# Kernel optimization log

Hardware: AMD Instinct MI355X
Metric: run time of the kernel (lower is better)

The kernel has to match this reference:

```python
import jax, jax.numpy as jnp
import numpy as np
import math

NH, NR, HD, QK, ITERS = 8, 8, 64, 32, 4


def _pe(seq_len, dim):
    n = 1.0 / (1.0 + math.exp(-1))
    pos = np.arange(seq_len, dtype=np.float64)[:, None]
    i = np.arange(0, dim, 2, dtype=np.float64)[None, :]
    pe = np.zeros((seq_len, dim), np.float32)
    pe[:, 0::2] = n * np.sin(pos / 10000 ** (2 * i / dim))
    pe[:, 1::2] = n * np.cos(pos / 10000 ** (2 * (i + 1) / dim))
    return jnp.asarray(pe)


def _ln(x, g, b, eps=1e-5):
    m = x.mean(-1, keepdims=True)
    v = ((x - m) ** 2).mean(-1, keepdims=True)
    return (x - m) * jax.lax.rsqrt(v + eps) * g + b


def _comp_attn(x, norm1_g, norm1_b, norm2_g, norm2_b, q_w, q_b, k_w, k_b,
               v_w, v_b, qv_w, qv_b, score_w, score_b, final_w, final_b,
               ffn1_w, ffn1_b, ffn2_w, ffn2_b):
    B, S, D = x.shape
    res = x
    h = _ln(x, norm1_g, norm1_b)
    q = (h @ q_w + q_b).reshape(B, S, NH, HD).transpose(0, 2, 1, 3) / math.sqrt(HD)  # [B,nh,S,hd]
    k = (h @ k_w + k_b).reshape(B, S, NH, HD)                                         # [B,S,nh,hd]
    v = (h @ v_w + v_b).reshape(B, S, NR, HD)                                         # [B,S,nr,hd]
    score = jax.nn.softmax(jnp.einsum('bhqd,bkhd->bhqk', q, k), axis=-1)              # [B,nh,S,S]
    out = jnp.einsum('bhqk,bkrd->bqhrd', score, v)                                    # [B,S,nh,nr,hd]
    qv = (h @ qv_w + qv_b).reshape(B, S, NH, QK)
    qv_e = jnp.broadcast_to(qv[:, :, :, None, :], (B, S, NH, NR, QK))
    in_ = jnp.concatenate([qv_e, out], axis=-1)                                       # [B,S,nh,nr,qk+hd]
    comp = jax.nn.softmax(in_ @ score_w + score_b, axis=3)                            # [B,S,nh,nr,1]
    o = (comp * out).sum(axis=3).reshape(B, S, D)
    o = o @ final_w + final_b
    x = res + o
    res2 = x
    h2 = _ln(x, norm2_g, norm2_b)
    ff = jax.nn.relu(h2 @ ffn1_w + ffn1_b) @ ffn2_w + ffn2_b  # dropout identity (eval)
    return res2 + ff


def reference(img, qst, conv_w, conv_b, qrep_w, qrep_b, cls_token, map_w, map_b,
              norm1_g, norm1_b, norm2_g, norm2_b, q_w, q_b, k_w, k_b, v_w, v_b,
              qv_w, qv_b, score_w, score_b, final_w, final_b,
              ffn1_w, ffn1_b, ffn2_w, ffn2_b, out_w, out_b):
    B = img.shape[0]
    H = conv_w.shape[0]  # 256
    pe = _pe(25, H)
    # patch embedding: conv 15x15 stride 15 -> [B,H,5,5]
    p = jax.lax.conv_general_dilated(img, conv_w, (15, 15), 'VALID',
                                     dimension_numbers=('NCHW', 'OIHW', 'NCHW'))
    p = p + conv_b[None, :, None, None]
    p = p.reshape(B, H, 25).transpose(0, 2, 1) + pe[None]       # [B,25,H]
    cls = jnp.broadcast_to(cls_token, (B, 1, H))
    emb = jnp.concatenate([cls, p], axis=1)                      # [B,26,H]
    que = (qst @ qrep_w + qrep_b)[:, None, :]
    que = jnp.broadcast_to(que, (B, 26, H))
    x = jnp.concatenate([emb, que], axis=-1)                     # [B,26,2H]
    x = x @ map_w + map_b                                        # [B,26,D]
    for _ in range(ITERS):
        x = _comp_attn(x, norm1_g, norm1_b, norm2_g, norm2_b, q_w, q_b, k_w, k_b,
                       v_w, v_b, qv_w, qv_b, score_w, score_b, final_w, final_b,
                       ffn1_w, ffn1_b, ffn2_w, ffn2_b)
    y = x[:, 0, :] @ out_w + out_b
    return jax.nn.log_softmax(y, axis=1)


def setup_inputs() -> dict:
    key = jax.random.key(0)
    ks = iter(jax.random.split(key, 64))
    def rn(shape, s=0.02):
        return jax.random.normal(next(ks), shape, jnp.float32) * s
    B, D, H = 256, 512, 256
    return {
        'img': jax.random.normal(next(ks), (B, 3, 75, 75), jnp.float32),
        'qst': jax.random.normal(next(ks), (B, 18), jnp.float32),
        'conv_w': rn((H, 3, 15, 15)), 'conv_b': rn((H,)),
        'qrep_w': rn((18, H)), 'qrep_b': rn((H,)),
        'cls_token': rn((1, 1, H), 1.0),
        'map_w': rn((2 * H, D)), 'map_b': rn((D,)),
        'norm1_g': jnp.ones((D,), jnp.float32), 'norm1_b': jnp.zeros((D,), jnp.float32),
        'norm2_g': jnp.ones((D,), jnp.float32), 'norm2_b': jnp.zeros((D,), jnp.float32),
        'q_w': rn((D, D)), 'q_b': rn((D,)),
        'k_w': rn((D, D)), 'k_b': rn((D,)),
        'v_w': rn((D, NR * HD)), 'v_b': rn((NR * HD,)),
        'qv_w': rn((D, QK * NH)), 'qv_b': rn((QK * NH,)),
        'score_w': rn((HD + QK, 1)), 'score_b': rn((1,)),
        'final_w': rn((D, D)), 'final_b': rn((D,)),
        'ffn1_w': rn((D, 2 * D)), 'ffn1_b': rn((2 * D,)),
        'ffn2_w': rn((2 * D, D)), 'ffn2_b': rn((D,)),
        'out_w': rn((D, 10)), 'out_b': rn((10,)),
    }
```

## Files before the change

kernel.cpp:

```cpp
#include <hip/hip_runtime.h>
#include <math.h>

#define NB 256
#define SEQ 26
#define TOK (NB*SEQ)
#define DIM 512

typedef unsigned short u16;
typedef __attribute__((ext_vector_type(8))) short short8_t;
typedef __attribute__((ext_vector_type(4))) float floatx4;

__device__ inline u16 f2bf(float f) {
    union { float f; unsigned u; } v; v.f = f;
    unsigned r = v.u + 0x7fffu + ((v.u >> 16) & 1u);
    return (u16)(r >> 16);
}
__device__ inline float bf2f(u16 u) {
    union { unsigned u; float f; } v; v.u = ((unsigned)u) << 16; return v.f;
}

__device__ __forceinline__ void gload_lds16(const u16* g, u16* l) {
    __builtin_amdgcn_global_load_lds((const __attribute__((address_space(1))) void*)g,
                                     (__attribute__((address_space(3))) void*)l, 16, 0, 0);
}

__global__ void prep_all(const float* __restrict__ q_w, const float* __restrict__ k_w,
                         const float* __restrict__ v_w, const float* __restrict__ final_w,
                         const float* __restrict__ ffn1_w, const float* __restrict__ ffn2_w,
                         const float* __restrict__ map_w, const float* __restrict__ conv_w,
                         const float* __restrict__ q_b, const float* __restrict__ k_b,
                         const float* __restrict__ v_b, const float* __restrict__ cls,
                         const float* __restrict__ qst, const float* __restrict__ qrep_w,
                         const float* __restrict__ qrep_b, const float* __restrict__ map_b,
                         u16* __restrict__ qkvT, u16* __restrict__ finT,
                         u16* __restrict__ f1T, u16* __restrict__ f2T,
                         u16* __restrict__ mapT, u16* __restrict__ cwT,
                         float* __restrict__ qkvb, u16* __restrict__ emb,
                         float* __restrict__ quem) {
    __shared__ float lds[64][65];
    __shared__ float que[256];
    int blk = blockIdx.x;
    int t = threadIdx.x;
    if (blk < 544) {
        const float* W; u16* Wt; int K, N, tbase;
        if (blk < 64)       { W = q_w;     Wt = qkvT;            K = 512;  N = 512;  tbase = 0;   }
        else if (blk < 128) { W = k_w;     Wt = qkvT + 512*512;  K = 512;  N = 512;  tbase = 64;  }
        else if (blk < 192) { W = v_w;     Wt = qkvT + 1024*512; K = 512;  N = 512;  tbase = 128; }
        else if (blk < 256) { W = final_w; Wt = finT;            K = 512;  N = 512;  tbase = 192; }
        else if (blk < 384) { W = ffn1_w;  Wt = f1T;             K = 512;  N = 1024; tbase = 256; }
        else if (blk < 512) { W = ffn2_w;  Wt = f2T;             K = 1024; N = 512;  tbase = 384; }
        else                { W = map_w;   Wt = mapT;            K = 256;  N = 512;  tbase = 512; }
        int tloc = blk - tbase;
        int ntn = N >> 6;
        int n0 = (tloc % ntn) * 64, k0 = (tloc / ntn) * 64;
        int j = t & 63, i0 = t >> 6;
        #pragma unroll
        for (int p = 0; p < 16; ++p) {
            int i = i0*16 + p;
            lds[i][j] = W[(size_t)(k0+i)*N + n0 + j];
        }
        __syncthreads();
        int i2 = t & 63, j0 = t >> 6;
        #pragma unroll
        for (int p = 0; p < 16; ++p) {
            int j2 = j0*16 + p;
            Wt[(size_t)(n0+j2)*K + k0 + i2] = f2bf(lds[i2][j2]);
        }
    } else if (blk < 800) {
        int oc = blk - 544;
        for (int jj = t; jj < 704; jj += 256)
            cwT[(size_t)oc*704 + jj] = (jj < 675) ? f2bf(conv_w[(size_t)oc*675 + jj]) : (u16)0;
    } else if (blk < 1056) {
        int b = blk - 800;
        emb[(size_t)(b*SEQ)*256 + t] = f2bf(cls[t]);
    } else if (blk == 1056) {
        for (int jj = t; jj < 1536; jj += 256)
            qkvb[jj] = jj < 512 ? q_b[jj] : (jj < 1024 ? k_b[jj-512] : v_b[jj-1024]);
    } else {
        int b = blk - 1057;
        float acc = qrep_b[t];
        for (int j = 0; j < 18; ++j) acc += qst[b*18 + j] * qrep_w[j*256 + t];
        que[t] = acc;
        __syncthreads();
        for (int n = t; n < DIM; n += 256) {
            float a2 = map_b[n];
            for (int k = 0; k < 256; ++k) a2 += que[k] * map_w[(256 + k)*DIM + n];
            quem[b*DIM + n] = a2;
        }
    }
}

__global__ void im2col_kernel(const float* __restrict__ img, u16* __restrict__ P) {
    int ri = blockIdx.x;
    int b = ri / 25, pos = ri % 25, ph = pos/5, pw = pos%5;
    for (int j = threadIdx.x; j < 704; j += 256) {
        float v = 0.f;
        if (j < 675) {
            int c = j / 225, rem = j % 225, kh = rem/15, kw = rem%15;
            v = img[(size_t)((b*3+c)*75 + ph*15 + kh)*75 + pw*15 + kw];
        }
        P[(size_t)ri*704 + j] = f2bf(v);
    }
}

template<int BM, int RESMODE, int RELU, int OUTBF>
__global__ __launch_bounds__(512) void mfma_gemm(const u16* __restrict__ A, const u16* __restrict__ Bt,
                          const float* __restrict__ bias, const void* __restrict__ res,
                          void* __restrict__ Cout, int M, int N, int K, float alpha) {
    constexpr int MI  = BM / 32;
    constexpr int ALD = BM / 64;
    __shared__ __align__(16) u16 As[2][BM*64];
    __shared__ __align__(16) u16 Bs[2][128*64];
    const int tid = threadIdx.x;
    const int lane = tid & 63;
    const int w = tid >> 6;
    const int wr = (w >> 2) * (MI*16);
    const int wc = (w & 3) * 32;
    const int bm = blockIdx.y * BM, bn = blockIdx.x * 128;

    floatx4 acc[MI][2];
    #pragma unroll
    for (int mi = 0; mi < MI; ++mi)
        #pragma unroll
        for (int ni = 0; ni < 2; ++ni)
            acc[mi][ni] = (floatx4){0.f,0.f,0.f,0.f};

    const u16* aptr[ALD];
    int aidx[ALD];
    #pragma unroll
    for (int s = 0; s < ALD; ++s) {
        int idx = s*512 + tid;
        int row = idx >> 3, ch = (idx & 7) ^ (row & 7);
        aptr[s] = &A[(size_t)(bm+row)*K + ch*8];
        aidx[s] = idx;
    }
    const u16* bptr[2];
    int bidx[2];
    #pragma unroll
    for (int s = 0; s < 2; ++s) {
        int idx = s*512 + tid;
        int row = idx >> 3, ch = (idx & 7) ^ (row & 7);
        bptr[s] = &Bt[(size_t)(bn+row)*K + ch*8];
        bidx[s] = idx;
    }

    const int nt = K >> 6;
    #pragma unroll
    for (int s = 0; s < ALD; ++s) gload_lds16(aptr[s], &As[0][aidx[s]*8]);
    #pragma unroll
    for (int s = 0; s < 2; ++s)   gload_lds16(bptr[s], &Bs[0][bidx[s]*8]);
    __syncthreads();

    for (int t = 0; t < nt; ++t) {
        const int cur = t & 1;
        if (t + 1 < nt) {
            int off = (t + 1) << 6;
            #pragma unroll
            for (int s = 0; s < ALD; ++s) gload_lds16(aptr[s] + off, &As[cur^1][aidx[s]*8]);
            #pragma unroll
            for (int s = 0; s < 2; ++s)   gload_lds16(bptr[s] + off, &Bs[cur^1][bidx[s]*8]);
        }
        #pragma unroll
        for (int kk = 0; kk < 2; ++kk) {
            int ch2 = kk*4 + (lane >> 4);
            short8_t af[MI], bf[2];
            #pragma unroll
            for (int mi = 0; mi < MI; ++mi) {
                int row = wr + mi*16 + (lane & 15);
                af[mi] = *(const short8_t*)&As[cur][row*64 + ((ch2 ^ (row & 7))*8)];
            }
            #pragma unroll
            for (int ni = 0; ni < 2; ++ni) {
                int rowb = wc + ni*16 + (lane & 15);
                bf[ni] = *(const short8_t*)&Bs[cur][rowb*64 + ((ch2 ^ (rowb & 7))*8)];
            }
            #pragma unroll
            for (int mi = 0; mi < MI; ++mi)
                #pragma unroll
                for (int ni = 0; ni < 2; ++ni)
                    acc[mi][ni] = __builtin_amdgcn_mfma_f32_16x16x32_bf16(
                        af[mi], bf[ni], acc[mi][ni], 0, 0, 0);
        }
        __syncthreads();
    }

    #pragma unroll
    for (int mi = 0; mi < MI; ++mi) {
        #pragma unroll
        for (int ni = 0; ni < 2; ++ni) {
            int col = bn + wc + ni*16 + (lane & 15);
            float bv = bias ? bias[col] : 0.0f;
            #pragma unroll
            for (int r = 0; r < 4; ++r) {
                int row = bm + wr + mi*16 + (lane >> 4)*4 + r;
                float v = (acc[mi][ni][r] + bv) * alpha;
                if (RELU) v = fmaxf(v, 0.f);
                if (RESMODE == 1)      v += bf2f(((const u16*)res)[(size_t)row*N + col]);
                else if (RESMODE == 2) v += ((const float*)res)[(size_t)(row/SEQ)*N + col];
                if (RESMODE == 3) {
                    int bb = row / 25, pos = row - bb*25;
                    float freq = __powf(10000.0f, -(float)col / 128.0f);
                    float a = (float)pos * freq;
                    float pe = 0.7310585786300049f * ((col & 1) ? __cosf(a) : __sinf(a));
                    ((u16*)Cout)[(size_t)(bb*SEQ + 1 + pos)*256 + col] = f2bf(v + pe);
                } else if (OUTBF) {
                    ((u16*)Cout)[(size_t)row*N + col] = f2bf(v);
                } else {
                    ((float*)Cout)[(size_t)row*N + col] = v;
                }
            }
        }
    }
}

__global__ void ln_kernel(const u16* __restrict__ x, const float* __restrict__ g,
                          const float* __restrict__ bta, u16* __restrict__ out) {
    int row = blockIdx.x * 4 + (threadIdx.x >> 6);
    int lane = threadIdx.x & 63;
    short8_t xin = *(const short8_t*)&x[(size_t)row*DIM + lane*8];
    float xv[8];
    #pragma unroll
    for (int j = 0; j < 8; ++j) xv[j] = bf2f((u16)xin[j]);
    float s = 0.f, sq = 0.f;
    #pragma unroll
    for (int j = 0; j < 8; ++j) { s += xv[j]; sq += xv[j]*xv[j]; }
    #pragma unroll
    for (int off = 32; off; off >>= 1) {
        s  += __shfl_xor(s,  off);
        sq += __shfl_xor(sq, off);
    }
    float m = s * (1.0f/DIM);
    float r = rsqrtf(sq * (1.0f/DIM) - m*m + 1e-5f);
    floatx4 g0 = *(const floatx4*)(g + lane*8);
    floatx4 g1 = *(const floatx4*)(g + lane*8 + 4);
    floatx4 b0 = *(const floatx4*)(bta + lane*8);
    floatx4 b1 = *(const floatx4*)(bta + lane*8 + 4);
    short8_t o;
    o[0] = (short)f2bf((xv[0]-m)*r*g0[0] + b0[0]);
    o[1] = (short)f2bf((xv[1]-m)*r*g0[1] + b0[1]);
    o[2] = (short)f2bf((xv[2]-m)*r*g0[2] + b0[2]);
    o[3] = (short)f2bf((xv[3]-m)*r*g0[3] + b0[3]);
    o[4] = (short)f2bf((xv[4]-m)*r*g1[0] + b1[0]);
    o[5] = (short)f2bf((xv[5]-m)*r*g1[1] + b1[1]);
    o[6] = (short)f2bf((xv[6]-m)*r*g1[2] + b1[2]);
    o[7] = (short)f2bf((xv[7]-m)*r*g1[3] + b1[3]);
    *(short8_t*)&out[(size_t)row*DIM + lane*8] = o;
}

__global__ __launch_bounds__(512) void attn_fused_kernel(const u16* __restrict__ qkv,
                                                         const float* __restrict__ score_w,
                                                         u16* __restrict__ attn_o) {
    int b = blockIdx.x;
    __shared__ u16 Bt[64*224];
    __shared__ float s_lds[208*28];
    __shared__ float vwl[208];
    __shared__ float cmp_lds[208*8];
    __shared__ float swl[64];
    int tid = threadIdx.x;
    int lane = tid & 63, w = tid >> 6;

    if (tid < 64) swl[tid] = score_w[32 + tid];
    for (int k = 0; k < 26; ++k) {
        int d2 = tid & 63, r = tid >> 6;
        u16 v = qkv[(size_t)(b*SEQ+k)*1536 + 1024 + tid];
        int bo = (d2*448 + (k*8+r)*2) ^ ((d2 & 7) << 4);
        *(u16*)((char*)Bt + bo) = v;
    }
    {
        int d2 = tid & 63, kr = 208 + (tid >> 6);
        int bo1 = (d2*448 + kr*2)     ^ ((d2 & 7) << 4);
        int bo2 = (d2*448 + (kr+8)*2) ^ ((d2 & 7) << 4);
        *(u16*)((char*)Bt + bo1) = 0;
        *(u16*)((char*)Bt + bo2) = 0;
    }
    for (int row = tid; row < 208; row += 512) {
        s_lds[row*28 + 26] = 0.f; s_lds[row*28 + 27] = 0.f;
    }

    {
        int h = w;
        int col16 = lane & 15, ch = lane >> 4;
        short8_t qf[2][2], kf[2][2];
        #pragma unroll
        for (int mi = 0; mi < 2; ++mi) {
            int q = mi*16 + col16;
            #pragma unroll
            for (int kk = 0; kk < 2; ++kk) {
                if (q < 26)
                    qf[mi][kk] = *(const short8_t*)&qkv[(size_t)(b*SEQ+q)*1536 + h*64 + kk*32 + ch*8];
                else
                    qf[mi][kk] = (short8_t){0,0,0,0,0,0,0,0};
            }
        }
        #pragma unroll
        for (int ni = 0; ni < 2; ++ni) {
            int kq = ni*16 + col16;
            #pragma unroll
            for (int kk = 0; kk < 2; ++kk) {
                if (kq < 26)
                    kf[ni][kk] = *(const short8_t*)&qkv[(size_t)(b*SEQ+kq)*1536 + 512 + h*64 + kk*32 + ch*8];
                else
                    kf[ni][kk] = (short8_t){0,0,0,0,0,0,0,0};
            }
        }
        floatx4 sacc[2][2];
        #pragma unroll
        for (int mi = 0; mi < 2; ++mi)
            #pragma unroll
            for (int ni = 0; ni < 2; ++ni)
                sacc[mi][ni] = (floatx4){0.f,0.f,0.f,0.f};
        #pragma unroll
        for (int kk = 0; kk < 2; ++kk)
            #pragma unroll
            for (int mi = 0; mi < 2; ++mi)
                #pragma unroll
                for (int ni = 0; ni < 2; ++ni)
                    sacc[mi][ni] = __builtin_amdgcn_mfma_f32_16x16x32_bf16(
                        qf[mi][kk], kf[ni][kk], sacc[mi][ni], 0, 0, 0);
        #pragma unroll
        for (int mi = 0; mi < 2; ++mi) {
            #pragma unroll
            for (int r = 0; r < 4; ++r) {
                float s0 = sacc[mi][0][r] * 0.125f;
                float s1 = (col16 < 10) ? sacc[mi][1][r] * 0.125f : -1e30f;
                float mx = fmaxf(s0, s1);
                #pragma unroll
                for (int msk = 1; msk < 16; msk <<= 1) mx = fmaxf(mx, __shfl_xor(mx, msk));
                float e0 = __expf(s0 - mx);
                float e1 = (col16 < 10) ? __expf(s1 - mx) : 0.f;
                float den = e0 + e1;
                #pragma unroll
                for (int msk = 1; msk < 16; msk <<= 1) den += __shfl_xor(den, msk);
                float inv = 1.f / den;
                int q = mi*16 + ch*4 + r;
                if (q < 26) {
                    s_lds[(h*26+q)*28 + col16] = e0 * inv;
                    if (col16 < 10) s_lds[(h*26+q)*28 + 16 + col16] = e1 * inv;
                }
            }
        }
    }
    __syncthreads();

    if (tid < 416) {
        int kr = tid >> 1, h0 = (tid & 1) * 32;
        float acc = 0.f;
        #pragma unroll
        for (int dd = 0; dd < 32; ++dd) {
            int d2 = h0 + dd;
            int bo = (d2*448 + kr*2) ^ ((d2 & 7) << 4);
            acc += bf2f(*(const u16*)((const char*)Bt + bo)) * swl[d2];
        }
        acc += __shfl_xor(acc, 1);
        if ((tid & 1) == 0) vwl[kr] = acc;
    }
    __syncthreads();

    if (tid < 208) {
        float srow[26];
        #pragma unroll
        for (int k = 0; k < 26; ++k) srow[k] = s_lds[tid*28 + k];
        float e[8];
        #pragma unroll
        for (int r = 0; r < 8; ++r) {
            float a = 0.f;
            #pragma unroll
            for (int k = 0; k < 26; ++k) a += srow[k] * vwl[k*8 + r];
            e[r] = a;
        }
        float m = e[0];
        #pragma unroll
        for (int r = 1; r < 8; ++r) m = fmaxf(m, e[r]);
        float den = 0.f;
        #pragma unroll
        for (int r = 0; r < 8; ++r) { e[r] = __expf(e[r]-m); den += e[r]; }
        float inv = 1.f/den;
        #pragma unroll
        for (int r = 0; r < 8; ++r) cmp_lds[tid*8+r] = e[r]*inv;
    }
    __syncthreads();

    int mh = w >> 2, nt = w & 3;
    int ntile0 = nt*16;
    short8_t bfr[7];
    #pragma unroll
    for (int ks = 0; ks < 7; ++ks) {
        int col = ntile0 + (lane & 15);
        int krb = ks*32 + (lane >> 4)*8;
        int bo = (col*448 + krb*2) ^ ((col & 7) << 4);
        bfr[ks] = *(const short8_t*)((const char*)Bt + bo);
    }
    int mt0 = mh ? 7 : 0, mt1 = mh ? 13 : 7;
    for (int mt = mt0; mt < mt1; ++mt) {
        int arow = mt*16 + (lane & 15);
        float c8[8];
        #pragma unroll
        for (int r = 0; r < 8; ++r) c8[r] = cmp_lds[arow*8 + r];
        floatx4 acc = (floatx4){0.f,0.f,0.f,0.f};
        #pragma unroll
        for (int ks = 0; ks < 7; ++ks) {
            int k = ks*4 + (lane >> 4);
            float sv = s_lds[arow*28 + k];
            short8_t af;
            #pragma unroll
            for (int j = 0; j < 8; ++j) af[j] = (short)f2bf(sv * c8[j]);
            acc = __builtin_amdgcn_mfma_f32_16x16x32_bf16(af, bfr[ks], acc, 0, 0, 0);
        }
        int colg = ntile0 + (lane & 15);
        #pragma unroll
        for (int rr = 0; rr < 4; ++rr) {
            int rowg = mt*16 + (lane >> 4)*4 + rr;
            int h = rowg / 26, q = rowg - h*26;
            attn_o[(size_t)(b*SEQ+q)*DIM + h*64 + colg] = f2bf(acc[rr]);
        }
    }
}

__global__ void head_kernel(const u16* __restrict__ x, const float* __restrict__ out_w,
                            const float* __restrict__ out_b, float* __restrict__ y) {
    int b = blockIdx.x;
    int tid = threadIdx.x;
    const u16* xr = x + (size_t)(b*SEQ)*DIM;
    float x0 = bf2f(xr[tid]), x1 = bf2f(xr[tid+256]);
    float part[10];
    #pragma unroll
    for (int c = 0; c < 10; ++c)
        part[c] = x0*out_w[tid*10 + c] + x1*out_w[(tid+256)*10 + c];
    #pragma unroll
    for (int off = 32; off; off >>= 1)
        #pragma unroll
        for (int c = 0; c < 10; ++c) part[c] += __shfl_down(part[c], off);
    __shared__ float red[4][10];
    __shared__ float yv[10];
    int wid = tid >> 6, lane = tid & 63;
    if (lane == 0)
        #pragma unroll
        for (int c = 0; c < 10; ++c) red[wid][c] = part[c];
    __syncthreads();
    if (tid < 10)
        yv[tid] = out_b[tid] + red[0][tid] + red[1][tid] + red[2][tid] + red[3][tid];
    __syncthreads();
    if (tid < 10) {
        float m = yv[0];
        #pragma unroll
        for (int i = 1; i < 10; ++i) m = fmaxf(m, yv[i]);
        float den = 0.0f;
        #pragma unroll
        for (int i = 0; i < 10; ++i) den += __expf(yv[i]-m);
        y[b*10 + tid] = yv[tid] - m - __logf(den);
    }
}

extern "C" void kernel_launch(void* const* d_in, const int* in_sizes, int n_in,
                              void* d_out, int out_size, void* d_ws, size_t ws_size,
                              hipStream_t stream) {
    const float* img      = (const float*)d_in[0];
    const float* qst      = (const float*)d_in[1];
    const float* conv_w   = (const float*)d_in[2];
    const float* conv_b   = (const float*)d_in[3];
    const float* qrep_w   = (const float*)d_in[4];
    const float* qrep_b   = (const float*)d_in[5];
    const float* cls_tok  = (const float*)d_in[6];
    const float* map_w    = (const float*)d_in[7];
    const float* map_b    = (const float*)d_in[8];
    const float* norm1_g  = (const float*)d_in[9];
    const float* norm1_b  = (const float*)d_in[10];
    const float* norm2_g  = (const float*)d_in[11];
    const float* norm2_b  = (const float*)d_in[12];
    const float* q_w      = (const float*)d_in[13];
    const float* q_b      = (const float*)d_in[14];
    const float* k_w      = (const float*)d_in[15];
    const float* k_b      = (const float*)d_in[16];
    const float* v_w      = (const float*)d_in[17];
    const float* v_b      = (const float*)d_in[18];
    const float* score_w  = (const float*)d_in[21];
    const float* final_w  = (const float*)d_in[23];
    const float* final_b  = (const float*)d_in[24];
    const float* ffn1_w   = (const float*)d_in[25];
    const float* ffn1_b   = (const float*)d_in[26];
    const float* ffn2_w   = (const float*)d_in[27];
    const float* ffn2_b   = (const float*)d_in[28];
    const float* out_w    = (const float*)d_in[29];
    const float* out_b    = (const float*)d_in[30];

    float* ws = (float*)d_ws;
    size_t o = 0;
    u16* x      = (u16*)(ws+o); o += (size_t)TOK*DIM/2;
    u16* qkvT   = (u16*)(ws+o); o += (size_t)1536*512/2;
    u16* finT   = (u16*)(ws+o); o += (size_t)512*512/2;
    u16* f1T    = (u16*)(ws+o); o += (size_t)1024*512/2;
    u16* f2T    = (u16*)(ws+o); o += (size_t)512*1024/2;
    u16* mapT   = (u16*)(ws+o); o += (size_t)512*256/2;
    u16* cwT    = (u16*)(ws+o); o += (size_t)256*704/2;
    float* qkvb = ws + o;       o += 1536;
    float* r2   = ws + o;
    u16*  h_bf    = (u16*)r2;
    u16*  qkv_bf  = (u16*)(r2 + (size_t)TOK*DIM/2);
    u16*  attn_obf= (u16*)(r2 + (size_t)TOK*DIM/2 + (size_t)TOK*1536/2);
    u16*  ffbuf   = qkv_bf;
    u16*  Pbuf    = (u16*)r2;
    u16*  emb_bf  = (u16*)(r2 + (size_t)6400*704/2);
    float* quem   = r2 + (size_t)6400*704/2 + (size_t)TOK*256/2;

    prep_all<<<1313, 256, 0, stream>>>(q_w, k_w, v_w, final_w, ffn1_w, ffn2_w, map_w, conv_w,
                                       q_b, k_b, v_b, cls_tok, qst, qrep_w, qrep_b, map_b,
                                       qkvT, finT, f1T, f2T, mapT, cwT, qkvb, emb_bf, quem);

    im2col_kernel<<<6400, 256, 0, stream>>>(img, Pbuf);
    mfma_gemm<64,3,0,1><<<dim3(2,100), dim3(512), 0, stream>>>(
        Pbuf, cwT, conv_b, nullptr, emb_bf, 6400, 256, 704, 1.0f);
    mfma_gemm<64,2,0,1><<<dim3(4,104), dim3(512), 0, stream>>>(
        emb_bf, mapT, nullptr, quem, x, TOK, 512, 256, 1.0f);

    for (int it = 0; it < 4; ++it) {
        ln_kernel<<<TOK/4, 256, 0, stream>>>(x, norm1_g, norm1_b, h_bf);
        mfma_gemm<128,0,0,1><<<dim3(12,52), dim3(512), 0, stream>>>(
            h_bf, qkvT, qkvb, nullptr, qkv_bf, TOK, 1536, 512, 1.0f);
        attn_fused_kernel<<<NB, 512, 0, stream>>>(qkv_bf, score_w, attn_obf);
        mfma_gemm<64,1,0,1><<<dim3(4,104), dim3(512), 0, stream>>>(
            attn_obf, finT, final_b, x, x, TOK, 512, 512, 1.0f);
        ln_kernel<<<TOK/4, 256, 0, stream>>>(x, norm2_g, norm2_b, h_bf);
        mfma_gemm<128,0,1,1><<<dim3(8,52), dim3(512), 0, stream>>>(
            h_bf, f1T, ffn1_b, nullptr, ffbuf, TOK, 1024, 512, 1.0f);
        mfma_gemm<64,1,0,1><<<dim3(4,104), dim3(512), 0, stream>>>(
            ffbuf, f2T, ffn2_b, x, x, TOK, 512, 1024, 1.0f);
    }

    head_kernel<<<NB, 256, 0, stream>>>(x, out_w, out_b, (float*)d_out);
}
```

Measured before the change: 510.2 us.

## Fuse final projection and residual add into attention kernel

The attention kernel now writes its per-batch output tile into shared memory (reusing the Bt region) instead of global memory. It then runs the 26x512x512 final projection with MFMA, adding the bias and residual directly into x. This removes a separate GEMM launch and the attn_o global round trip. In exchange, each of the 256 blocks streams the full finT weight from global/L2 without LDS staging and pads 26 rows to 32, which may make the projection less efficient than the tiled GEMM.

```diff
diff --git a/kernel.cpp b/kernel.cpp
--- a/kernel.cpp
+++ b/kernel.cpp
@@ -249,13 +249,17 @@
 
 __global__ __launch_bounds__(512) void attn_fused_kernel(const u16* __restrict__ qkv,
                                                          const float* __restrict__ score_w,
-                                                         u16* __restrict__ attn_o) {
+                                                         const u16* __restrict__ finT,
+                                                         const float* __restrict__ final_b,
+                                                         u16* __restrict__ x) {
     int b = blockIdx.x;
-    __shared__ u16 Bt[64*224];
-    __shared__ float s_lds[208*28];
-    __shared__ float vwl[208];
-    __shared__ float cmp_lds[208*8];
-    __shared__ float swl[64];
+    __shared__ __align__(16) char smem[59712];
+    char*  Btc     = smem;
+    float* s_lds   = (float*)(smem + 28672);
+    float* vwl     = (float*)(smem + 51968);
+    float* cmp_lds = (float*)(smem + 52800);
+    float* swl     = (float*)(smem + 59456);
+    u16*   A_lds   = (u16*)smem;
     int tid = threadIdx.x;
     int lane = tid & 63, w = tid >> 6;
 
@@ -264,14 +268,14 @@
         int d2 = tid & 63, r = tid >> 6;
         u16 v = qkv[(size_t)(b*SEQ+k)*1536 + 1024 + tid];
         int bo = (d2*448 + (k*8+r)*2) ^ ((d2 & 7) << 4);
-        *(u16*)((char*)Bt + bo) = v;
+        *(u16*)(Btc + bo) = v;
     }
     {
         int d2 = tid & 63, kr = 208 + (tid >> 6);
         int bo1 = (d2*448 + kr*2)     ^ ((d2 & 7) << 4);
         int bo2 = (d2*448 + (kr+8)*2) ^ ((d2 & 7) << 4);
-        *(u16*)((char*)Bt + bo1) = 0;
-        *(u16*)((char*)Bt + bo2) = 0;
+        *(u16*)(Btc + bo1) = 0;
+        *(u16*)(Btc + bo2) = 0;
     }
     for (int row = tid; row < 208; row += 512) {
         s_lds[row*28 + 26] = 0.f; s_lds[row*28 + 27] = 0.f;
@@ -349,7 +353,7 @@
         for (int dd = 0; dd < 32; ++dd) {
             int d2 = h0 + dd;
             int bo = (d2*448 + kr*2) ^ ((d2 & 7) << 4);
-            acc += bf2f(*(const u16*)((const char*)Bt + bo)) * swl[d2];
+            acc += bf2f(*(const u16*)(Btc + bo)) * swl[d2];
         }
         acc += __shfl_xor(acc, 1);
         if ((tid & 1) == 0) vwl[kr] = acc;
@@ -388,10 +392,14 @@
         int col = ntile0 + (lane & 15);
         int krb = ks*32 + (lane >> 4)*8;
         int bo = (col*448 + krb*2) ^ ((col & 7) << 4);
-        bfr[ks] = *(const short8_t*)((const char*)Bt + bo);
+        bfr[ks] = *(const short8_t*)(Btc + bo);
     }
     int mt0 = mh ? 7 : 0, mt1 = mh ? 13 : 7;
-    for (int mt = mt0; mt < mt1; ++mt) {
+    floatx4 oacc[7];
+    #pragma unroll
+    for (int oi = 0; oi < 7; ++oi) {
+        int mt = mt0 + oi;
+        if (mt >= mt1) break;
         int arow = mt*16 + (lane & 15);
         float c8[8];
         #pragma unroll
@@ -406,12 +414,72 @@
             for (int j = 0; j < 8; ++j) af[j] = (short)f2bf(sv * c8[j]);
             acc = __builtin_amdgcn_mfma_f32_16x16x32_bf16(af, bfr[ks], acc, 0, 0, 0);
         }
-        int colg = ntile0 + (lane & 15);
+        oacc[oi] = acc;
+    }
+    __syncthreads();
+
+    for (int idx = tid; idx < 6*512; idx += 512) {
+        int r_ = 26 + (idx >> 9), c_ = idx & 511;
+        int bo = (r_*1024 + c_*2) ^ ((r_ & 7) << 4);
+        *(u16*)((char*)A_lds + bo) = 0;
+    }
+    #pragma unroll
+    for (int oi = 0; oi < 7; ++oi) {
+        int mt = mt0 + oi;
+        if (mt >= mt1) break;
         #pragma unroll
         for (int rr = 0; rr < 4; ++rr) {
             int rowg = mt*16 + (lane >> 4)*4 + rr;
             int h = rowg / 26, q = rowg - h*26;
-            attn_o[(size_t)(b*SEQ+q)*DIM + h*64 + colg] = f2bf(acc[rr]);
+            int k = h*64 + ntile0 + (lane & 15);
+            int bo = (q*1024 + k*2) ^ ((q & 7) << 4);
+            *(u16*)((char*)A_lds + bo) = f2bf(oacc[oi][rr]);
+        }
+    }
+    __syncthreads();
+
+    int n0 = w * 64;
+    floatx4 facc[2][4];
+    #pragma unroll
+    for (int mi = 0; mi < 2; ++mi)
+        #pragma unroll
+        for (int ni = 0; ni < 4; ++ni)
+            facc[mi][ni] = (floatx4){0.f,0.f,0.f,0.f};
+    for (int ks = 0; ks < 16; ++ks) {
+        int kchunk = ks*32 + (lane >> 4)*8;
+        short8_t af[2], bfv[4];
+        #pragma unroll
+        for (int mi = 0; mi < 2; ++mi) {
+            int r_ = mi*16 + (lane & 15);
+            int bo = (r_*1024 + kchunk*2) ^ ((r_ & 7) << 4);
+            af[mi] = *(const short8_t*)((const char*)A_lds + bo);
+        }
+        #pragma unroll
+        for (int ni = 0; ni < 4; ++ni) {
+            int n = n0 + ni*16 + (lane & 15);
+            bfv[ni] = *(const short8_t*)&finT[(size_t)n*512 + kchunk];
+        }
+        #pragma unroll
+        for (int mi = 0; mi < 2; ++mi)
+            #pragma unroll
+            for (int ni = 0; ni < 4; ++ni)
+                facc[mi][ni] = __builtin_amdgcn_mfma_f32_16x16x32_bf16(
+                    af[mi], bfv[ni], facc[mi][ni], 0, 0, 0);
+    }
+    #pragma unroll
+    for (int mi = 0; mi < 2; ++mi) {
+        #pragma unroll
+        for (int ni = 0; ni < 4; ++ni) {
+            int n = n0 + ni*16 + (lane & 15);
+            #pragma unroll
+            for (int r = 0; r < 4; ++r) {
+                int q = mi*16 + (lane >> 4)*4 + r;
+                if (q < 26) {
+                    size_t off = (size_t)(b*SEQ+q)*DIM + n;
+                    float v = facc[mi][ni][r] + final_b[n] + bf2f(x[off]);
+                    x[off] = f2bf(v);
+                }
+            }
         }
     }
 }
@@ -496,7 +564,6 @@
     float* r2   = ws + o;
     u16*  h_bf    = (u16*)r2;
     u16*  qkv_bf  = (u16*)(r2 + (size_t)TOK*DIM/2);
-    u16*  attn_obf= (u16*)(r2 + (size_t)TOK*DIM/2 + (size_t)TOK*1536/2);
     u16*  ffbuf   = qkv_bf;
     u16*  Pbuf    = (u16*)r2;
     u16*  emb_bf  = (u16*)(r2 + (size_t)6400*704/2);
@@ -516,9 +583,7 @@
         ln_kernel<<<TOK/4, 256, 0, stream>>>(x, norm1_g, norm1_b, h_bf);
         mfma_gemm<128,0,0,1><<<dim3(12,52), dim3(512), 0, stream>>>(
             h_bf, qkvT, qkvb, nullptr, qkv_bf, TOK, 1536, 512, 1.0f);
-        attn_fused_kernel<<<NB, 512, 0, stream>>>(qkv_bf, score_w, attn_obf);
-        mfma_gemm<64,1,0,1><<<dim3(4,104), dim3(512), 0, stream>>>(
-            attn_obf, finT, final_b, x, x, TOK, 512, 512, 1.0f);
+        attn_fused_kernel<<<NB, 512, 0, stream>>>(qkv_bf, score_w, finT, final_b, x);
         ln_kernel<<<TOK/4, 256, 0, stream>>>(x, norm2_g, norm2_b, h_bf);
         mfma_gemm<128,0,1,1><<<dim3(8,52), dim3(512), 0, stream>>>(
             h_bf, f1T, ffn1_b, nullptr, ffbuf, TOK, 1024, 512, 1.0f);
```

Result: slower. 547.0 us (+7.2%).
